# Optimization experiments

Measured on AMD Instinct MI355X. Metric: run time of the kernel, lower is better.

Reference implementation:

```python
import jax, jax.numpy as jnp
import numpy as np

N = 100000
D = 16          # input_dim
NUM_FILTERS = 8
NNZ = 1600000


def setup_inputs() -> dict:
    key = jax.random.key(0)
    k1, k2, k3, k4, k5 = jax.random.split(key, 5)
    x = jax.random.normal(k1, (N, D), dtype=jnp.float32)
    L_rows = jax.random.randint(k2, (NNZ,), 0, N, dtype=jnp.int64 if jax.config.jax_enable_x64 else jnp.int32).astype(jnp.int32)
    L_cols = jax.random.randint(k3, (NNZ,), 0, N, dtype=jnp.int32)
    L_v = jax.random.normal(k4, (NNZ,), dtype=jnp.float32)
    node_attr_eig = jax.random.uniform(k5, (N,), dtype=jnp.float32)
    return {"x": x, "L_rows": L_rows, "L_cols": L_cols, "L_v": L_v, "node_attr_eig": node_attr_eig}


def reference(x, L_rows, L_cols, L_v, node_attr_eig):
    n, d = x.shape
    f = NUM_FILTERS
    # exponents = 2 ** arange(num_filters + 1)
    exponents = (2 ** jnp.arange(f + 1)).astype(x.dtype)  # [F+1]
    # coeffs = x.T @ L  ==  (L.T @ x).T ; compute L.T @ x as [N, D]
    # (L.T @ x)[c] = sum over nnz entries (r, c): L_v * x[r]
    LTx = jax.ops.segment_sum(L_v[:, None] * x[L_rows], L_cols, num_segments=n)  # [N, D]
    # exponential eigenfilter bank: w = exp(-eig)^exponents, wavelet differences
    w = jnp.exp(-node_attr_eig)[:, None] ** exponents[None, :]  # [N, F+1]
    w_wav = w[:, :-1] - w[:, 1:]                                # [N, F]
    # g_eig = coeffs[..., None] * w_wav[None, ...] permuted to [N, D, F]
    g_eig = (LTx[:, :, None] * w_wav[:, None, :]).reshape(n, d * f)  # [N, D*F]
    # filtered = L @ g_eig : out[r] = sum over nnz (r, c): L_v * g_eig[c]
    out = jax.ops.segment_sum(L_v[:, None] * g_eig[L_cols], L_rows, num_segments=n)
    return out.reshape(n, d, f)
```

## Files before the change

kernel.cpp:

```cpp
#include <hip/hip_runtime.h>

#define N_NODES   100000
#define D_DIM     16
#define NFILT     8
#define KOUT      128
#define NNZ_CNT   1600000

#define SHIFT1    12
#define NC1       25
#define CAP1      67072
#define NSUB      64
#define CROWS     64
#define NCB       (NC1 * NSUB)
#define CAP       1408
#define EPB       2048
#define NBLKA     ((NNZ_CNT + EPB - 1) / EPB)
#define CHB       ((CAP1 + EPB - 1) / EPB)
#define CPAD      16


__device__ __forceinline__ uint f32_to_bf16_bits(float f) {
    uint u = __float_as_uint(f);
    uint r = (u + 0x7FFFu + ((u >> 16) & 1u)) >> 16;
    return r;
}

__global__ void wav_kernel(const float* __restrict__ eig, uint* __restrict__ combo) {
    int n = blockIdx.x * blockDim.x + threadIdx.x;
    if (n >= N_NODES) return;
    float cur = expf(-eig[n]);
    uint pk[4];
#pragma unroll
    for (int h = 0; h < 4; ++h) {
        float nx0 = cur * cur;
        float w0 = cur - nx0;
        float nx1 = nx0 * nx0;
        float w1 = nx0 - nx1;
        cur = nx1;
        pk[h] = f32_to_bf16_bits(w0) | (f32_to_bf16_bits(w1) << 16);
    }
    *(uint4*)(combo + (size_t)n * 16 + 8) = make_uint4(pk[0], pk[1], pk[2], pk[3]);
}

__global__ __launch_bounds__(512) void binC2_kernel(const int* __restrict__ rows,
                                                    const int* __restrict__ cols,
                                                    const float* __restrict__ v,
                                                    int* __restrict__ gc1c,
                                                    int* __restrict__ gc1r,
                                                    int2* __restrict__ regBc,
                                                    int2* __restrict__ regBr) {
    __shared__ int cnt[NC1], offb[NC1], gbase[NC1], cur[NC1];
    __shared__ int2 rec[EPB];
    __shared__ unsigned char rbk[EPB];
    int tid = threadIdx.x;
    int e0 = blockIdx.x * EPB;
    int nE = NNZ_CNT - e0; if (nE > EPB) nE = EPB;

    int r_[4], c_[4], vb_[4];
    int nk = 0;
#pragma unroll
    for (int kk = 0; kk < 4; ++kk) {
        int i = tid + kk * 512;
        if (i < nE) {
            r_[kk] = rows[e0 + i];
            c_[kk] = cols[e0 + i];
            vb_[kk] = __float_as_int(v[e0 + i]);
            nk = kk + 1;
        }
    }

    if (tid < NC1) cnt[tid] = 0;
    __syncthreads();
    for (int kk = 0; kk < nk; ++kk) atomicAdd(&cnt[c_[kk] >> SHIFT1], 1);
    __syncthreads();
    if (tid == 0) { int run = 0; for (int b = 0; b < NC1; ++b) { offb[b] = run; run += cnt[b]; } }
    __syncthreads();
    if (tid < NC1) {
        gbase[tid] = cnt[tid] ? atomicAdd(&gc1c[tid * CPAD], cnt[tid]) : 0;
        cur[tid] = offb[tid];
    }
    __syncthreads();
    for (int kk = 0; kk < nk; ++kk) {
        int b = c_[kk] >> SHIFT1;
        int pos = atomicAdd(&cur[b], 1);
        rec[pos] = make_int2(((c_[kk] & 4095) << 17) | r_[kk], vb_[kk]);
        rbk[pos] = (unsigned char)b;
    }
    __syncthreads();
    for (int i = tid; i < nE; i += 512) {
        int b = rbk[i];
        int slot = gbase[b] + (i - offb[b]);
        if (slot < CAP1) regBc[(size_t)b * CAP1 + slot] = rec[i];
    }
    __syncthreads();

    if (tid < NC1) cnt[tid] = 0;
    __syncthreads();
    for (int kk = 0; kk < nk; ++kk) atomicAdd(&cnt[r_[kk] >> SHIFT1], 1);
    __syncthreads();
    if (tid == 0) { int run = 0; for (int b = 0; b < NC1; ++b) { offb[b] = run; run += cnt[b]; } }
    __syncthreads();
    if (tid < NC1) {
        gbase[tid] = cnt[tid] ? atomicAdd(&gc1r[tid * CPAD], cnt[tid]) : 0;
        cur[tid] = offb[tid];
    }
    __syncthreads();
    for (int kk = 0; kk < nk; ++kk) {
        int b = r_[kk] >> SHIFT1;
        int pos = atomicAdd(&cur[b], 1);
        rec[pos] = make_int2(((r_[kk] & 4095) << 17) | c_[kk], vb_[kk]);
        rbk[pos] = (unsigned char)b;
    }
    __syncthreads();
    for (int i = tid; i < nE; i += 512) {
        int b = rbk[i];
        int slot = gbase[b] + (i - offb[b]);
        if (slot < CAP1) regBr[(size_t)b * CAP1 + slot] = rec[i];
    }
}

__global__ __launch_bounds__(512) void binF_kernel(const int* __restrict__ gcur1,
                                                   const int2* __restrict__ regB,
                                                   int* __restrict__ gcurF,
                                                   int2* __restrict__ regA) {
    __shared__ int cnt[NSUB], offb[NSUB], gbase[NSUB], cur[NSUB];
    __shared__ int2 rec[EPB];
    __shared__ unsigned char rbk[EPB];
    int tid = threadIdx.x;
    int cb = blockIdx.x / CHB;
    int ch = blockIdx.x % CHB;
    int nc = gcur1[cb * CPAD]; if (nc > CAP1) nc = CAP1;
    int cs = ch * EPB;
    if (cs >= nc) return;
    int nE = nc - cs; if (nE > EPB) nE = EPB;
    size_t srcb = (size_t)cb * CAP1 + cs;

    if (tid < NSUB) cnt[tid] = 0;
    __syncthreads();

    int2 my[4]; int msub[4];
    int nk = 0;
#pragma unroll
    for (int kk = 0; kk < 4; ++kk) {
        int i = tid + kk * 512;
        msub[kk] = -1;
        if (i < nE) {
            my[kk] = regB[srcb + i];
            msub[kk] = (my[kk].x >> 23) & (NSUB - 1);
            nk = kk + 1;
            atomicAdd(&cnt[msub[kk]], 1);
        }
    }
    __syncthreads();

    if (tid == 0) { int run = 0; for (int b = 0; b < NSUB; ++b) { offb[b] = run; run += cnt[b]; } }
    __syncthreads();
    if (tid < NSUB) {
        gbase[tid] = cnt[tid] ? atomicAdd(&gcurF[(cb * NSUB + tid) * CPAD], cnt[tid]) : 0;
        cur[tid] = offb[tid];
    }
    __syncthreads();

    for (int kk = 0; kk < nk; ++kk)
        if (msub[kk] >= 0) {
            int pos = atomicAdd(&cur[msub[kk]], 1);
            rec[pos] = make_int2(my[kk].x & 0x7FFFFF, my[kk].y);
            rbk[pos] = (unsigned char)msub[kk];
        }
    __syncthreads();

    for (int i = tid; i < nE; i += 512) {
        int b = rbk[i];
        int slot = gbase[b] + (i - offb[b]);
        if (slot < CAP)
            regA[(size_t)(cb * NSUB + b) * CAP + slot] = rec[i];
    }
}

__global__ __launch_bounds__(256) void sortgather1_kernel(const int* __restrict__ gcurF,
                                                          const int2* __restrict__ regA,
                                                          const float* __restrict__ x,
                                                          uint* __restrict__ combo) {
    __shared__ int2 rec[CAP];
    __shared__ int cnt[CROWS], sc[CROWS], st[CROWS], cur[CROWS];
    int tid = threadIdx.x;
    int b = blockIdx.x;
    int nb = gcurF[b * CPAD]; if (nb > CAP) nb = CAP;
    size_t base = (size_t)b * CAP;

    int2 my[6]; int mkey[6];
    if (tid < CROWS) cnt[tid] = 0;
    __syncthreads();
#pragma unroll
    for (int s = 0; s < 6; ++s) {
        int i = tid + s * 256;
        mkey[s] = -1;
        if (i < nb) {
            my[s] = regA[base + i];
            mkey[s] = my[s].x >> 17;
            atomicAdd(&cnt[mkey[s]], 1);
        }
    }
    __syncthreads();

    int cv = (tid < CROWS) ? cnt[tid] : 0;
    if (tid < CROWS) sc[tid] = cv;
    __syncthreads();
    for (int off = 1; off < CROWS; off <<= 1) {
        int t = (tid < CROWS && tid >= off) ? sc[tid - off] : 0;
        __syncthreads();
        if (tid < CROWS) sc[tid] += t;
        __syncthreads();
    }
    if (tid < CROWS) { int s0 = sc[tid] - cv; st[tid] = s0; cur[tid] = s0; }
    __syncthreads();

#pragma unroll
    for (int s = 0; s < 6; ++s)
        if (mkey[s] >= 0) {
            int pos = atomicAdd(&cur[mkey[s]], 1);
            if (pos < CAP) rec[pos] = make_int2(my[s].x & 0x1FFFF, my[s].y);
        }
    __syncthreads();

    int wave = tid >> 6, lane = tid & 63;
    int d = lane & 15, j = lane >> 4;
    for (int cl = wave; cl < CROWS; cl += 4) {
        int c = b * CROWS + cl;
        int i0 = st[cl], e0 = i0 + cnt[cl]; if (e0 > CAP) e0 = CAP;
        float acc = 0.f;
        for (int i = i0 + j; i < e0; i += 4) {
            int2 e = rec[i];
            acc = fmaf(__int_as_float(e.y), x[(size_t)e.x * D_DIM + d], acc);
        }
        acc += __shfl_xor(acc, 16);
        acc += __shfl_xor(acc, 32);
        float hi = __shfl_down(acc, 8);
        if (lane < 8 && c < N_NODES)
            combo[(size_t)c * 16 + lane] =
                f32_to_bf16_bits(acc) | (f32_to_bf16_bits(hi) << 16);
    }
}

__global__ __launch_bounds__(256) void sortgather2_kernel(const int* __restrict__ gcurF,
                                                          const int2* __restrict__ regA,
                                                          const uint* __restrict__ combo,
                                                          float* __restrict__ out) {
    __shared__ int2 rec[CAP];
    __shared__ int cnt[CROWS], sc[CROWS], st[CROWS], cur[CROWS];
    int tid = threadIdx.x;
    int b = blockIdx.x;
    int nb = gcurF[b * CPAD]; if (nb > CAP) nb = CAP;
    size_t base = (size_t)b * CAP;

    int2 my[6]; int mkey[6];
    if (tid < CROWS) cnt[tid] = 0;
    __syncthreads();
#pragma unroll
    for (int s = 0; s < 6; ++s) {
        int i = tid + s * 256;
        mkey[s] = -1;
        if (i < nb) {
            my[s] = regA[base + i];
            mkey[s] = my[s].x >> 17;
            atomicAdd(&cnt[mkey[s]], 1);
        }
    }
    __syncthreads();

    int cv = (tid < CROWS) ? cnt[tid] : 0;
    if (tid < CROWS) sc[tid] = cv;
    __syncthreads();
    for (int off = 1; off < CROWS; off <<= 1) {
        int t = (tid < CROWS && tid >= off) ? sc[tid - off] : 0;
        __syncthreads();
        if (tid < CROWS) sc[tid] += t;
        __syncthreads();
    }
    if (tid < CROWS) { int s0 = sc[tid] - cv; st[tid] = s0; cur[tid] = s0; }
    __syncthreads();

#pragma unroll
    for (int s = 0; s < 6; ++s)
        if (mkey[s] >= 0) {
            int pos = atomicAdd(&cur[mkey[s]], 1);
            if (pos < CAP) rec[pos] = make_int2(my[s].x & 0x1FFFF, my[s].y);
        }
    __syncthreads();

    int wave = tid >> 6, lane = tid & 63;
    int d0 = lane >> 3;
    int f  = lane & 7;
    for (int rl = wave; rl < CROWS; rl += 4) {
        int row = b * CROWS + rl;
        if (row >= N_NODES) continue;
        int i = st[rl], end = st[rl] + cnt[rl]; if (end > CAP) end = CAP;
        float acc0 = 0.f, acc1 = 0.f;
        for (; i + 4 <= end; i += 4) {
            int2 e0 = rec[i], e1 = rec[i + 1], e2 = rec[i + 2], e3 = rec[i + 3];
            uint l0 = combo[(size_t)e0.x * 16 + d0];
            uint l1 = combo[(size_t)e1.x * 16 + d0];
            uint l2 = combo[(size_t)e2.x * 16 + d0];
            uint l3 = combo[(size_t)e3.x * 16 + d0];
            uint w0 = ((const ushort*)(combo + (size_t)e0.x * 16 + 8))[f];
            uint w1 = ((const ushort*)(combo + (size_t)e1.x * 16 + 8))[f];
            uint w2 = ((const ushort*)(combo + (size_t)e2.x * 16 + 8))[f];
            uint w3 = ((const ushort*)(combo + (size_t)e3.x * 16 + 8))[f];
            float vw0 = __int_as_float(e0.y) * __uint_as_float(w0 << 16);
            float vw1 = __int_as_float(e1.y) * __uint_as_float(w1 << 16);
            float vw2 = __int_as_float(e2.y) * __uint_as_float(w2 << 16);
            float vw3 = __int_as_float(e3.y) * __uint_as_float(w3 << 16);
            acc0 = fmaf(vw0, __uint_as_float(l0 << 16), acc0);
            acc1 = fmaf(vw0, __uint_as_float(l0 & 0xFFFF0000u), acc1);
            acc0 = fmaf(vw1, __uint_as_float(l1 << 16), acc0);
            acc1 = fmaf(vw1, __uint_as_float(l1 & 0xFFFF0000u), acc1);
            acc0 = fmaf(vw2, __uint_as_float(l2 << 16), acc0);
            acc1 = fmaf(vw2, __uint_as_float(l2 & 0xFFFF0000u), acc1);
            acc0 = fmaf(vw3, __uint_as_float(l3 << 16), acc0);
            acc1 = fmaf(vw3, __uint_as_float(l3 & 0xFFFF0000u), acc1);
        }
        for (; i < end; ++i) {
            int2 e = rec[i];
            uint l = combo[(size_t)e.x * 16 + d0];
            uint w = ((const ushort*)(combo + (size_t)e.x * 16 + 8))[f];
            float vw = __int_as_float(e.y) * __uint_as_float(w << 16);
            acc0 = fmaf(vw, __uint_as_float(l << 16), acc0);
            acc1 = fmaf(vw, __uint_as_float(l & 0xFFFF0000u), acc1);
        }
        __builtin_nontemporal_store(acc0, &out[(size_t)row * KOUT + lane]);
        __builtin_nontemporal_store(acc1, &out[(size_t)row * KOUT + 64 + lane]);
    }
}

extern "C" void kernel_launch(void* const* d_in, const int* in_sizes, int n_in,
                              void* d_out, int out_size, void* d_ws, size_t ws_size,
                              hipStream_t stream) {
    const float* x      = (const float*)d_in[0];
    const int*   L_rows = (const int*)  d_in[1];
    const int*   L_cols = (const int*)  d_in[2];
    const float* L_v    = (const float*)d_in[3];
    const float* eig    = (const float*)d_in[4];
    float* out = (float*)d_out;

    uint* combo = (uint*)d_ws;
    int2* regBc = (int2*)(combo + (size_t)N_NODES * 16);
    int2* regBr = regBc + (size_t)NC1 * CAP1;
    int2* regA  = regBr + (size_t)NC1 * CAP1;
    int*  gc1c  = (int*)(regA + (size_t)NCB * CAP);
    int*  gc1r  = gc1c + NC1 * CPAD;
    int*  gfc   = gc1r + NC1 * CPAD;
    int*  gfr   = gfc + NCB * CPAD;

    hipMemsetAsync(gc1c, 0, (size_t)(2 * NC1 + 2 * NCB) * CPAD * sizeof(int), stream);

    wav_kernel<<<(N_NODES + 255) / 256, 256, 0, stream>>>(eig, combo);

    binC2_kernel<<<NBLKA, 512, 0, stream>>>(L_rows, L_cols, L_v, gc1c, gc1r, regBc, regBr);

    binF_kernel<<<NC1 * CHB, 512, 0, stream>>>(gc1c, regBc, gfc, regA);
    sortgather1_kernel<<<NCB, 256, 0, stream>>>(gfc, regA, x, combo);

    binF_kernel<<<NC1 * CHB, 512, 0, stream>>>(gc1r, regBr, gfr, regA);
    sortgather2_kernel<<<NCB, 256, 0, stream>>>(gfr, regA, combo, out);
}
```

Before: 260.0 us.

## Fuse wavelet into binning and co-schedule row binning with first gather

Moves the eigen-wavelet computation into the first binning kernel, removing a separate launch. It gives the column and row fine-binning passes separate scratch buffers, so the row-side fine binning can run in the same launch as the first sort-gather. That merged launch uses 512-thread blocks with a shared-memory union, which is meant to cut launch gaps and let the two independent stages overlap. It also shrinks the per-bucket capacity from 1408 to 1280, which lowers shared memory and register use but raises the risk of dropping entries if a bucket overflows.

```diff
diff --git a/kernel.cpp b/kernel.cpp
--- a/kernel.cpp
+++ b/kernel.cpp
@@ -12,11 +12,14 @@
 #define NSUB      64
 #define CROWS     64
 #define NCB       (NC1 * NSUB)
-#define CAP       1408
+#define CAP       1280
 #define EPB       2048
 #define NBLKA     ((NNZ_CNT + EPB - 1) / EPB)
 #define CHB       ((CAP1 + EPB - 1) / EPB)
+#define NBF       (NC1 * CHB)
 #define CPAD      16
+
+#define SMEM_INTS 4864
 
 
 __device__ __forceinline__ uint f32_to_bf16_bits(float f) {
@@ -25,36 +28,39 @@
     return r;
 }
 
-__global__ void wav_kernel(const float* __restrict__ eig, uint* __restrict__ combo) {
-    int n = blockIdx.x * blockDim.x + threadIdx.x;
-    if (n >= N_NODES) return;
-    float cur = expf(-eig[n]);
-    uint pk[4];
-#pragma unroll
-    for (int h = 0; h < 4; ++h) {
-        float nx0 = cur * cur;
-        float w0 = cur - nx0;
-        float nx1 = nx0 * nx0;
-        float w1 = nx0 - nx1;
-        cur = nx1;
-        pk[h] = f32_to_bf16_bits(w0) | (f32_to_bf16_bits(w1) << 16);
-    }
-    *(uint4*)(combo + (size_t)n * 16 + 8) = make_uint4(pk[0], pk[1], pk[2], pk[3]);
-}
-
 __global__ __launch_bounds__(512) void binC2_kernel(const int* __restrict__ rows,
                                                     const int* __restrict__ cols,
                                                     const float* __restrict__ v,
+                                                    const float* __restrict__ eig,
                                                     int* __restrict__ gc1c,
                                                     int* __restrict__ gc1r,
                                                     int2* __restrict__ regBc,
-                                                    int2* __restrict__ regBr) {
+                                                    int2* __restrict__ regBr,
+                                                    uint* __restrict__ combo) {
     __shared__ int cnt[NC1], offb[NC1], gbase[NC1], cur[NC1];
     __shared__ int2 rec[EPB];
     __shared__ unsigned char rbk[EPB];
     int tid = threadIdx.x;
     int e0 = blockIdx.x * EPB;
     int nE = NNZ_CNT - e0; if (nE > EPB) nE = EPB;
+
+    {
+        int n = blockIdx.x * 128 + tid;
+        if (tid < 128 && n < N_NODES) {
+            float curw = expf(-eig[n]);
+            uint pk[4];
+#pragma unroll
+            for (int h = 0; h < 4; ++h) {
+                float nx0 = curw * curw;
+                float w0 = curw - nx0;
+                float nx1 = nx0 * nx0;
+                float w1 = nx0 - nx1;
+                curw = nx1;
+                pk[h] = f32_to_bf16_bits(w0) | (f32_to_bf16_bits(w1) << 16);
+            }
+            *(uint4*)(combo + (size_t)n * 16 + 8) = make_uint4(pk[0], pk[1], pk[2], pk[3]);
+        }
+    }
 
     int r_[4], c_[4], vb_[4];
     int nk = 0;
@@ -119,16 +125,21 @@
     }
 }
 
-__global__ __launch_bounds__(512) void binF_kernel(const int* __restrict__ gcur1,
-                                                   const int2* __restrict__ regB,
-                                                   int* __restrict__ gcurF,
-                                                   int2* __restrict__ regA) {
-    __shared__ int cnt[NSUB], offb[NSUB], gbase[NSUB], cur[NSUB];
-    __shared__ int2 rec[EPB];
-    __shared__ unsigned char rbk[EPB];
+__device__ __forceinline__ void binF_body(int bfb,
+                                          const int* __restrict__ gcur1,
+                                          const int2* __restrict__ regB,
+                                          int* __restrict__ gcurF,
+                                          int2* __restrict__ regA,
+                                          int* sm) {
+    int* cnt   = sm;
+    int* offb  = sm + NSUB;
+    int* gbase = sm + 2 * NSUB;
+    int* cur   = sm + 3 * NSUB;
+    int2* rec  = (int2*)(sm + 256);
+    unsigned char* rbk = (unsigned char*)(sm + 256 + 2 * EPB);
     int tid = threadIdx.x;
-    int cb = blockIdx.x / CHB;
-    int ch = blockIdx.x % CHB;
+    int cb = bfb / CHB;
+    int ch = bfb % CHB;
     int nc = gcur1[cb * CPAD]; if (nc > CAP1) nc = CAP1;
     int cs = ch * EPB;
     if (cs >= nc) return;
@@ -177,23 +188,35 @@
     }
 }
 
-__global__ __launch_bounds__(256) void sortgather1_kernel(const int* __restrict__ gcurF,
-                                                          const int2* __restrict__ regA,
-                                                          const float* __restrict__ x,
-                                                          uint* __restrict__ combo) {
-    __shared__ int2 rec[CAP];
-    __shared__ int cnt[CROWS], sc[CROWS], st[CROWS], cur[CROWS];
+__global__ __launch_bounds__(512) void binF_kernel(const int* __restrict__ gcur1,
+                                                   const int2* __restrict__ regB,
+                                                   int* __restrict__ gcurF,
+                                                   int2* __restrict__ regA) {
+    __shared__ alignas(16) int sm[SMEM_INTS];
+    binF_body(blockIdx.x, gcur1, regB, gcurF, regA, sm);
+}
+
+__device__ __forceinline__ void sg1_body(int b,
+                                         const int* __restrict__ gcurF,
+                                         const int2* __restrict__ regA,
+                                         const float* __restrict__ x,
+                                         uint* __restrict__ combo,
+                                         int* sm) {
+    int* cnt = sm;
+    int* sc  = sm + CROWS;
+    int* st  = sm + 2 * CROWS;
+    int* cur = sm + 3 * CROWS;
+    int2* rec = (int2*)(sm + 256);
     int tid = threadIdx.x;
-    int b = blockIdx.x;
     int nb = gcurF[b * CPAD]; if (nb > CAP) nb = CAP;
     size_t base = (size_t)b * CAP;
 
-    int2 my[6]; int mkey[6];
+    int2 my[3]; int mkey[3];
     if (tid < CROWS) cnt[tid] = 0;
     __syncthreads();
 #pragma unroll
-    for (int s = 0; s < 6; ++s) {
-        int i = tid + s * 256;
+    for (int s = 0; s < 3; ++s) {
+        int i = tid + s * 512;
         mkey[s] = -1;
         if (i < nb) {
             my[s] = regA[base + i];
@@ -216,7 +239,7 @@
     __syncthreads();
 
 #pragma unroll
-    for (int s = 0; s < 6; ++s)
+    for (int s = 0; s < 3; ++s)
         if (mkey[s] >= 0) {
             int pos = atomicAdd(&cur[mkey[s]], 1);
             if (pos < CAP) rec[pos] = make_int2(my[s].x & 0x1FFFF, my[s].y);
@@ -225,7 +248,7 @@
 
     int wave = tid >> 6, lane = tid & 63;
     int d = lane & 15, j = lane >> 4;
-    for (int cl = wave; cl < CROWS; cl += 4) {
+    for (int cl = wave; cl < CROWS; cl += 8) {
         int c = b * CROWS + cl;
         int i0 = st[cl], e0 = i0 + cnt[cl]; if (e0 > CAP) e0 = CAP;
         float acc = 0.f;
@@ -240,6 +263,20 @@
             combo[(size_t)c * 16 + lane] =
                 f32_to_bf16_bits(acc) | (f32_to_bf16_bits(hi) << 16);
     }
+}
+
+__global__ __launch_bounds__(512) void binFr_sg1_kernel(const int* __restrict__ gc1r,
+                                                        const int2* __restrict__ regBr,
+                                                        int* __restrict__ gfr,
+                                                        int2* __restrict__ regAr,
+                                                        const int* __restrict__ gfc,
+                                                        const int2* __restrict__ regAc,
+                                                        const float* __restrict__ x,
+                                                        uint* __restrict__ combo) {
+    __shared__ alignas(16) int sm[SMEM_INTS];
+    int bb = blockIdx.x;
+    if (bb < NBF) binF_body(bb, gc1r, regBr, gfr, regAr, sm);
+    else          sg1_body(bb - NBF, gfc, regAc, x, combo, sm);
 }
 
 __global__ __launch_bounds__(256) void sortgather2_kernel(const int* __restrict__ gcurF,
@@ -253,11 +290,11 @@
     int nb = gcurF[b * CPAD]; if (nb > CAP) nb = CAP;
     size_t base = (size_t)b * CAP;
 
-    int2 my[6]; int mkey[6];
+    int2 my[5]; int mkey[5];
     if (tid < CROWS) cnt[tid] = 0;
     __syncthreads();
 #pragma unroll
-    for (int s = 0; s < 6; ++s) {
+    for (int s = 0; s < 5; ++s) {
         int i = tid + s * 256;
         mkey[s] = -1;
         if (i < nb) {
@@ -281,7 +318,7 @@
     __syncthreads();
 
 #pragma unroll
-    for (int s = 0; s < 6; ++s)
+    for (int s = 0; s < 5; ++s)
         if (mkey[s] >= 0) {
             int pos = atomicAdd(&cur[mkey[s]], 1);
             if (pos < CAP) rec[pos] = make_int2(my[s].x & 0x1FFFF, my[s].y);
@@ -345,21 +382,22 @@
     uint* combo = (uint*)d_ws;
     int2* regBc = (int2*)(combo + (size_t)N_NODES * 16);
     int2* regBr = regBc + (size_t)NC1 * CAP1;
-    int2* regA  = regBr + (size_t)NC1 * CAP1;
-    int*  gc1c  = (int*)(regA + (size_t)NCB * CAP);
+    int2* regAc = regBr + (size_t)NC1 * CAP1;
+    int2* regAr = regAc + (size_t)NCB * CAP;
+    int*  gc1c  = (int*)(regAr + (size_t)NCB * CAP);
     int*  gc1r  = gc1c + NC1 * CPAD;
     int*  gfc   = gc1r + NC1 * CPAD;
     int*  gfr   = gfc + NCB * CPAD;
 
     hipMemsetAsync(gc1c, 0, (size_t)(2 * NC1 + 2 * NCB) * CPAD * sizeof(int), stream);
 
-    wav_kernel<<<(N_NODES + 255) / 256, 256, 0, stream>>>(eig, combo);
-
-    binC2_kernel<<<NBLKA, 512, 0, stream>>>(L_rows, L_cols, L_v, gc1c, gc1r, regBc, regBr);
-
-    binF_kernel<<<NC1 * CHB, 512, 0, stream>>>(gc1c, regBc, gfc, regA);
-    sortgather1_kernel<<<NCB, 256, 0, stream>>>(gfc, regA, x, combo);
-
-    binF_kernel<<<NC1 * CHB, 512, 0, stream>>>(gc1r, regBr, gfr, regA);
-    sortgather2_kernel<<<NCB, 256, 0, stream>>>(gfr, regA, combo, out);
-}
+    binC2_kernel<<<NBLKA, 512, 0, stream>>>(L_rows, L_cols, L_v, eig,
+                                            gc1c, gc1r, regBc, regBr, combo);
+
+    binF_kernel<<<NBF, 512, 0, stream>>>(gc1c, regBc, gfc, regAc);
+
+    binFr_sg1_kernel<<<NBF + NCB, 512, 0, stream>>>(gc1r, regBr, gfr, regAr,
+                                                    gfc, regAc, x, combo);
+
+    sortgather2_kernel<<<NCB, 256, 0, stream>>>(gfr, regAr, combo, out);
+}
```

Result: slower. 276.7 us (+6.4%).

## Use per-wave histograms in binning and replace sort-gather with shared-atomic accumulation

Applied to the files above, without the earlier changes.

The first binning kernel now builds a separate shared-memory histogram and scatter cursor for each wave, which cuts contention on the 25 shared counters. The first gather kernel no longer sorts edges by column inside the block. It accumulates each edge's contribution directly into a shared 64x16 float buffer with shared atomics, then packs the result to bf16. This removes the count, scan and scatter passes, but adds float atomic traffic and makes the summation order nondeterministic.

```diff
diff --git a/kernel.cpp b/kernel.cpp
--- a/kernel.cpp
+++ b/kernel.cpp
@@ -16,6 +16,7 @@
 #define EPB       2048
 #define NBLKA     ((NNZ_CNT + EPB - 1) / EPB)
 #define CHB       ((CAP1 + EPB - 1) / EPB)
+#define NWAVES    8
 #define CPAD      16
 
 
@@ -49,10 +50,12 @@
                                                     int* __restrict__ gc1r,
                                                     int2* __restrict__ regBc,
                                                     int2* __restrict__ regBr) {
-    __shared__ int cnt[NC1], offb[NC1], gbase[NC1], cur[NC1];
+    __shared__ int hist[NWAVES * NC1];
+    __shared__ int cnt[NC1], offb[NC1], gbase[NC1];
     __shared__ int2 rec[EPB];
     __shared__ unsigned char rbk[EPB];
     int tid = threadIdx.x;
+    int wv = tid >> 6;
     int e0 = blockIdx.x * EPB;
     int nE = NNZ_CNT - e0; if (nE > EPB) nE = EPB;
 
@@ -69,20 +72,32 @@
         }
     }
 
-    if (tid < NC1) cnt[tid] = 0;
-    __syncthreads();
-    for (int kk = 0; kk < nk; ++kk) atomicAdd(&cnt[c_[kk] >> SHIFT1], 1);
+    for (int i = tid; i < NWAVES * NC1; i += 512) hist[i] = 0;
+    __syncthreads();
+    for (int kk = 0; kk < nk; ++kk)
+        atomicAdd(&hist[wv * NC1 + (c_[kk] >> SHIFT1)], 1);
+    __syncthreads();
+    if (tid < NC1) {
+        int tot = 0;
+        for (int w = 0; w < NWAVES; ++w) tot += hist[w * NC1 + tid];
+        cnt[tid] = tot;
+    }
     __syncthreads();
     if (tid == 0) { int run = 0; for (int b = 0; b < NC1; ++b) { offb[b] = run; run += cnt[b]; } }
     __syncthreads();
     if (tid < NC1) {
         gbase[tid] = cnt[tid] ? atomicAdd(&gc1c[tid * CPAD], cnt[tid]) : 0;
-        cur[tid] = offb[tid];
+        int run = offb[tid];
+        for (int w = 0; w < NWAVES; ++w) {
+            int h = hist[w * NC1 + tid];
+            hist[w * NC1 + tid] = run;
+            run += h;
+        }
     }
     __syncthreads();
     for (int kk = 0; kk < nk; ++kk) {
         int b = c_[kk] >> SHIFT1;
-        int pos = atomicAdd(&cur[b], 1);
+        int pos = atomicAdd(&hist[wv * NC1 + b], 1);
         rec[pos] = make_int2(((c_[kk] & 4095) << 17) | r_[kk], vb_[kk]);
         rbk[pos] = (unsigned char)b;
     }
@@ -94,20 +109,32 @@
     }
     __syncthreads();
 
-    if (tid < NC1) cnt[tid] = 0;
-    __syncthreads();
-    for (int kk = 0; kk < nk; ++kk) atomicAdd(&cnt[r_[kk] >> SHIFT1], 1);
+    for (int i = tid; i < NWAVES * NC1; i += 512) hist[i] = 0;
+    __syncthreads();
+    for (int kk = 0; kk < nk; ++kk)
+        atomicAdd(&hist[wv * NC1 + (r_[kk] >> SHIFT1)], 1);
+    __syncthreads();
+    if (tid < NC1) {
+        int tot = 0;
+        for (int w = 0; w < NWAVES; ++w) tot += hist[w * NC1 + tid];
+        cnt[tid] = tot;
+    }
     __syncthreads();
     if (tid == 0) { int run = 0; for (int b = 0; b < NC1; ++b) { offb[b] = run; run += cnt[b]; } }
     __syncthreads();
     if (tid < NC1) {
         gbase[tid] = cnt[tid] ? atomicAdd(&gc1r[tid * CPAD], cnt[tid]) : 0;
-        cur[tid] = offb[tid];
+        int run = offb[tid];
+        for (int w = 0; w < NWAVES; ++w) {
+            int h = hist[w * NC1 + tid];
+            hist[w * NC1 + tid] = run;
+            run += h;
+        }
     }
     __syncthreads();
     for (int kk = 0; kk < nk; ++kk) {
         int b = r_[kk] >> SHIFT1;
-        int pos = atomicAdd(&cur[b], 1);
+        int pos = atomicAdd(&hist[wv * NC1 + b], 1);
         rec[pos] = make_int2(((r_[kk] & 4095) << 17) | c_[kk], vb_[kk]);
         rbk[pos] = (unsigned char)b;
     }
@@ -177,68 +204,40 @@
     }
 }
 
-__global__ __launch_bounds__(256) void sortgather1_kernel(const int* __restrict__ gcurF,
-                                                          const int2* __restrict__ regA,
-                                                          const float* __restrict__ x,
-                                                          uint* __restrict__ combo) {
+__global__ __launch_bounds__(256) void sg1_nosort_kernel(const int* __restrict__ gcurF,
+                                                         const int2* __restrict__ regA,
+                                                         const float* __restrict__ x,
+                                                         uint* __restrict__ combo) {
+    __shared__ float acc[CROWS * D_DIM];
     __shared__ int2 rec[CAP];
-    __shared__ int cnt[CROWS], sc[CROWS], st[CROWS], cur[CROWS];
     int tid = threadIdx.x;
     int b = blockIdx.x;
     int nb = gcurF[b * CPAD]; if (nb > CAP) nb = CAP;
     size_t base = (size_t)b * CAP;
 
-    int2 my[6]; int mkey[6];
-    if (tid < CROWS) cnt[tid] = 0;
-    __syncthreads();
-#pragma unroll
-    for (int s = 0; s < 6; ++s) {
-        int i = tid + s * 256;
-        mkey[s] = -1;
-        if (i < nb) {
-            my[s] = regA[base + i];
-            mkey[s] = my[s].x >> 17;
-            atomicAdd(&cnt[mkey[s]], 1);
-        }
-    }
-    __syncthreads();
-
-    int cv = (tid < CROWS) ? cnt[tid] : 0;
-    if (tid < CROWS) sc[tid] = cv;
-    __syncthreads();
-    for (int off = 1; off < CROWS; off <<= 1) {
-        int t = (tid < CROWS && tid >= off) ? sc[tid - off] : 0;
-        __syncthreads();
-        if (tid < CROWS) sc[tid] += t;
-        __syncthreads();
-    }
-    if (tid < CROWS) { int s0 = sc[tid] - cv; st[tid] = s0; cur[tid] = s0; }
-    __syncthreads();
-
-#pragma unroll
-    for (int s = 0; s < 6; ++s)
-        if (mkey[s] >= 0) {
-            int pos = atomicAdd(&cur[mkey[s]], 1);
-            if (pos < CAP) rec[pos] = make_int2(my[s].x & 0x1FFFF, my[s].y);
-        }
-    __syncthreads();
-
-    int wave = tid >> 6, lane = tid & 63;
-    int d = lane & 15, j = lane >> 4;
-    for (int cl = wave; cl < CROWS; cl += 4) {
+    for (int t = tid; t < CROWS * D_DIM; t += 256) acc[t] = 0.f;
+    for (int i = tid; i < nb; i += 256) rec[i] = regA[base + i];
+    __syncthreads();
+
+    int wv = tid >> 6, lane = tid & 63;
+    int sub = lane >> 4;
+    int d = lane & 15;
+    for (int i = (wv << 2) + sub; i < nb; i += 16) {
+        int2 e = rec[i];
+        int cl = e.x >> 17;
+        int r  = e.x & 0x1FFFF;
+        atomicAdd(&acc[(cl << 4) + d],
+                  __int_as_float(e.y) * x[(size_t)r * D_DIM + d]);
+    }
+    __syncthreads();
+
+    for (int t = tid; t < CROWS * NFILT; t += 256) {
+        int cl = t >> 3, j = t & 7;
         int c = b * CROWS + cl;
-        int i0 = st[cl], e0 = i0 + cnt[cl]; if (e0 > CAP) e0 = CAP;
-        float acc = 0.f;
-        for (int i = i0 + j; i < e0; i += 4) {
-            int2 e = rec[i];
-            acc = fmaf(__int_as_float(e.y), x[(size_t)e.x * D_DIM + d], acc);
-        }
-        acc += __shfl_xor(acc, 16);
-        acc += __shfl_xor(acc, 32);
-        float hi = __shfl_down(acc, 8);
-        if (lane < 8 && c < N_NODES)
-            combo[(size_t)c * 16 + lane] =
-                f32_to_bf16_bits(acc) | (f32_to_bf16_bits(hi) << 16);
+        if (c < N_NODES)
+            combo[(size_t)c * 16 + j] =
+                f32_to_bf16_bits(acc[(cl << 4) + j]) |
+                (f32_to_bf16_bits(acc[(cl << 4) + j + 8]) << 16);
     }
 }
 
@@ -358,7 +357,7 @@
     binC2_kernel<<<NBLKA, 512, 0, stream>>>(L_rows, L_cols, L_v, gc1c, gc1r, regBc, regBr);
 
     binF_kernel<<<NC1 * CHB, 512, 0, stream>>>(gc1c, regBc, gfc, regA);
-    sortgather1_kernel<<<NCB, 256, 0, stream>>>(gfc, regA, x, combo);
+    sg1_nosort_kernel<<<NCB, 256, 0, stream>>>(gfc, regA, x, combo);
 
     binF_kernel<<<NC1 * CHB, 512, 0, stream>>>(gc1r, regBr, gfr, regA);
     sortgather2_kernel<<<NCB, 256, 0, stream>>>(gfr, regA, combo, out);
```

New measurement: 376.0 us. +44.6%, slower.

## Use per-wave shared histograms in binning and split combo buffer into separate arrays

Applied to the files above, without the earlier changes.

The first binning kernel now keeps one histogram per wave and prefix-scans it per wave. Only 25 buckets are shared among 512 threads, so the single shared histogram's atomics were heavily contended; per-wave copies reduce that. The interleaved 64-byte combo record (LTx plus wavelet weights) is also split into two contiguous arrays, LTxP (32 B per node) and wavb (16 B per node). This changes the gather access pattern in the second sort-gather kernel, which may touch two cache lines per neighbor instead of one.

```diff
diff --git a/kernel.cpp b/kernel.cpp
--- a/kernel.cpp
+++ b/kernel.cpp
@@ -16,8 +16,8 @@
 #define EPB       2048
 #define NBLKA     ((NNZ_CNT + EPB - 1) / EPB)
 #define CHB       ((CAP1 + EPB - 1) / EPB)
+#define NWAVES    8
 #define CPAD      16
-
 
 __device__ __forceinline__ uint f32_to_bf16_bits(float f) {
     uint u = __float_as_uint(f);
@@ -25,7 +25,7 @@
     return r;
 }
 
-__global__ void wav_kernel(const float* __restrict__ eig, uint* __restrict__ combo) {
+__global__ void wav_kernel(const float* __restrict__ eig, ushort* __restrict__ wavb) {
     int n = blockIdx.x * blockDim.x + threadIdx.x;
     if (n >= N_NODES) return;
     float cur = expf(-eig[n]);
@@ -39,7 +39,7 @@
         cur = nx1;
         pk[h] = f32_to_bf16_bits(w0) | (f32_to_bf16_bits(w1) << 16);
     }
-    *(uint4*)(combo + (size_t)n * 16 + 8) = make_uint4(pk[0], pk[1], pk[2], pk[3]);
+    *(uint4*)(wavb + (size_t)n * NFILT) = make_uint4(pk[0], pk[1], pk[2], pk[3]);
 }
 
 __global__ __launch_bounds__(512) void binC2_kernel(const int* __restrict__ rows,
@@ -49,10 +49,12 @@
                                                     int* __restrict__ gc1r,
                                                     int2* __restrict__ regBc,
                                                     int2* __restrict__ regBr) {
-    __shared__ int cnt[NC1], offb[NC1], gbase[NC1], cur[NC1];
+    __shared__ int hist[NWAVES * NC1];
+    __shared__ int cnt[NC1], offb[NC1], gbase[NC1];
     __shared__ int2 rec[EPB];
     __shared__ unsigned char rbk[EPB];
     int tid = threadIdx.x;
+    int wv = tid >> 6;
     int e0 = blockIdx.x * EPB;
     int nE = NNZ_CNT - e0; if (nE > EPB) nE = EPB;
 
@@ -69,20 +71,32 @@
         }
     }
 
-    if (tid < NC1) cnt[tid] = 0;
-    __syncthreads();
-    for (int kk = 0; kk < nk; ++kk) atomicAdd(&cnt[c_[kk] >> SHIFT1], 1);
+    for (int i = tid; i < NWAVES * NC1; i += 512) hist[i] = 0;
+    __syncthreads();
+    for (int kk = 0; kk < nk; ++kk)
+        atomicAdd(&hist[wv * NC1 + (c_[kk] >> SHIFT1)], 1);
+    __syncthreads();
+    if (tid < NC1) {
+        int tot = 0;
+        for (int w = 0; w < NWAVES; ++w) tot += hist[w * NC1 + tid];
+        cnt[tid] = tot;
+    }
     __syncthreads();
     if (tid == 0) { int run = 0; for (int b = 0; b < NC1; ++b) { offb[b] = run; run += cnt[b]; } }
     __syncthreads();
     if (tid < NC1) {
         gbase[tid] = cnt[tid] ? atomicAdd(&gc1c[tid * CPAD], cnt[tid]) : 0;
-        cur[tid] = offb[tid];
+        int run = offb[tid];
+        for (int w = 0; w < NWAVES; ++w) {
+            int h = hist[w * NC1 + tid];
+            hist[w * NC1 + tid] = run;
+            run += h;
+        }
     }
     __syncthreads();
     for (int kk = 0; kk < nk; ++kk) {
         int b = c_[kk] >> SHIFT1;
-        int pos = atomicAdd(&cur[b], 1);
+        int pos = atomicAdd(&hist[wv * NC1 + b], 1);
         rec[pos] = make_int2(((c_[kk] & 4095) << 17) | r_[kk], vb_[kk]);
         rbk[pos] = (unsigned char)b;
     }
@@ -94,20 +108,32 @@
     }
     __syncthreads();
 
-    if (tid < NC1) cnt[tid] = 0;
-    __syncthreads();
-    for (int kk = 0; kk < nk; ++kk) atomicAdd(&cnt[r_[kk] >> SHIFT1], 1);
+    for (int i = tid; i < NWAVES * NC1; i += 512) hist[i] = 0;
+    __syncthreads();
+    for (int kk = 0; kk < nk; ++kk)
+        atomicAdd(&hist[wv * NC1 + (r_[kk] >> SHIFT1)], 1);
+    __syncthreads();
+    if (tid < NC1) {
+        int tot = 0;
+        for (int w = 0; w < NWAVES; ++w) tot += hist[w * NC1 + tid];
+        cnt[tid] = tot;
+    }
     __syncthreads();
     if (tid == 0) { int run = 0; for (int b = 0; b < NC1; ++b) { offb[b] = run; run += cnt[b]; } }
     __syncthreads();
     if (tid < NC1) {
         gbase[tid] = cnt[tid] ? atomicAdd(&gc1r[tid * CPAD], cnt[tid]) : 0;
-        cur[tid] = offb[tid];
+        int run = offb[tid];
+        for (int w = 0; w < NWAVES; ++w) {
+            int h = hist[w * NC1 + tid];
+            hist[w * NC1 + tid] = run;
+            run += h;
+        }
     }
     __syncthreads();
     for (int kk = 0; kk < nk; ++kk) {
         int b = r_[kk] >> SHIFT1;
-        int pos = atomicAdd(&cur[b], 1);
+        int pos = atomicAdd(&hist[wv * NC1 + b], 1);
         rec[pos] = make_int2(((r_[kk] & 4095) << 17) | c_[kk], vb_[kk]);
         rbk[pos] = (unsigned char)b;
     }
@@ -180,7 +206,7 @@
 __global__ __launch_bounds__(256) void sortgather1_kernel(const int* __restrict__ gcurF,
                                                           const int2* __restrict__ regA,
                                                           const float* __restrict__ x,
-                                                          uint* __restrict__ combo) {
+                                                          uint* __restrict__ LTxP) {
     __shared__ int2 rec[CAP];
     __shared__ int cnt[CROWS], sc[CROWS], st[CROWS], cur[CROWS];
     int tid = threadIdx.x;
@@ -237,14 +263,15 @@
         acc += __shfl_xor(acc, 32);
         float hi = __shfl_down(acc, 8);
         if (lane < 8 && c < N_NODES)
-            combo[(size_t)c * 16 + lane] =
+            LTxP[(size_t)c * NFILT + lane] =
                 f32_to_bf16_bits(acc) | (f32_to_bf16_bits(hi) << 16);
     }
 }
 
 __global__ __launch_bounds__(256) void sortgather2_kernel(const int* __restrict__ gcurF,
                                                           const int2* __restrict__ regA,
-                                                          const uint* __restrict__ combo,
+                                                          const uint* __restrict__ LTxP,
+                                                          const ushort* __restrict__ wavb,
                                                           float* __restrict__ out) {
     __shared__ int2 rec[CAP];
     __shared__ int cnt[CROWS], sc[CROWS], st[CROWS], cur[CROWS];
@@ -298,14 +325,14 @@
         float acc0 = 0.f, acc1 = 0.f;
         for (; i + 4 <= end; i += 4) {
             int2 e0 = rec[i], e1 = rec[i + 1], e2 = rec[i + 2], e3 = rec[i + 3];
-            uint l0 = combo[(size_t)e0.x * 16 + d0];
-            uint l1 = combo[(size_t)e1.x * 16 + d0];
-            uint l2 = combo[(size_t)e2.x * 16 + d0];
-            uint l3 = combo[(size_t)e3.x * 16 + d0];
-            uint w0 = ((const ushort*)(combo + (size_t)e0.x * 16 + 8))[f];
-            uint w1 = ((const ushort*)(combo + (size_t)e1.x * 16 + 8))[f];
-            uint w2 = ((const ushort*)(combo + (size_t)e2.x * 16 + 8))[f];
-            uint w3 = ((const ushort*)(combo + (size_t)e3.x * 16 + 8))[f];
+            uint l0 = LTxP[e0.x * NFILT + d0];
+            uint l1 = LTxP[e1.x * NFILT + d0];
+            uint l2 = LTxP[e2.x * NFILT + d0];
+            uint l3 = LTxP[e3.x * NFILT + d0];
+            uint w0 = wavb[e0.x * NFILT + f];
+            uint w1 = wavb[e1.x * NFILT + f];
+            uint w2 = wavb[e2.x * NFILT + f];
+            uint w3 = wavb[e3.x * NFILT + f];
             float vw0 = __int_as_float(e0.y) * __uint_as_float(w0 << 16);
             float vw1 = __int_as_float(e1.y) * __uint_as_float(w1 << 16);
             float vw2 = __int_as_float(e2.y) * __uint_as_float(w2 << 16);
@@ -321,8 +348,8 @@
         }
         for (; i < end; ++i) {
             int2 e = rec[i];
-            uint l = combo[(size_t)e.x * 16 + d0];
-            uint w = ((const ushort*)(combo + (size_t)e.x * 16 + 8))[f];
+            uint l = LTxP[e.x * NFILT + d0];
+            uint w = wavb[e.x * NFILT + f];
             float vw = __int_as_float(e.y) * __uint_as_float(w << 16);
             acc0 = fmaf(vw, __uint_as_float(l << 16), acc0);
             acc1 = fmaf(vw, __uint_as_float(l & 0xFFFF0000u), acc1);
@@ -342,24 +369,25 @@
     const float* eig    = (const float*)d_in[4];
     float* out = (float*)d_out;
 
-    uint* combo = (uint*)d_ws;
-    int2* regBc = (int2*)(combo + (size_t)N_NODES * 16);
-    int2* regBr = regBc + (size_t)NC1 * CAP1;
-    int2* regA  = regBr + (size_t)NC1 * CAP1;
-    int*  gc1c  = (int*)(regA + (size_t)NCB * CAP);
-    int*  gc1r  = gc1c + NC1 * CPAD;
-    int*  gfc   = gc1r + NC1 * CPAD;
-    int*  gfr   = gfc + NCB * CPAD;
+    uint*   LTxP = (uint*)d_ws;
+    ushort* wavb = (ushort*)(LTxP + (size_t)N_NODES * NFILT);
+    int2*   regBc = (int2*)(wavb + (size_t)N_NODES * NFILT);
+    int2*   regBr = regBc + (size_t)NC1 * CAP1;
+    int2*   regA  = regBr + (size_t)NC1 * CAP1;
+    int*    gc1c  = (int*)(regA + (size_t)NCB * CAP);
+    int*    gc1r  = gc1c + NC1 * CPAD;
+    int*    gfc   = gc1r + NC1 * CPAD;
+    int*    gfr   = gfc + NCB * CPAD;
 
     hipMemsetAsync(gc1c, 0, (size_t)(2 * NC1 + 2 * NCB) * CPAD * sizeof(int), stream);
 
-    wav_kernel<<<(N_NODES + 255) / 256, 256, 0, stream>>>(eig, combo);
+    wav_kernel<<<(N_NODES + 255) / 256, 256, 0, stream>>>(eig, wavb);
 
     binC2_kernel<<<NBLKA, 512, 0, stream>>>(L_rows, L_cols, L_v, gc1c, gc1r, regBc, regBr);
 
     binF_kernel<<<NC1 * CHB, 512, 0, stream>>>(gc1c, regBc, gfc, regA);
-    sortgather1_kernel<<<NCB, 256, 0, stream>>>(gfc, regA, x, combo);
+    sortgather1_kernel<<<NCB, 256, 0, stream>>>(gfc, regA, x, LTxP);
 
     binF_kernel<<<NC1 * CHB, 512, 0, stream>>>(gc1r, regBr, gfr, regA);
-    sortgather2_kernel<<<NCB, 256, 0, stream>>>(gfr, regA, combo, out);
-}
+    sortgather2_kernel<<<NCB, 256, 0, stream>>>(gfr, regA, LTxP, wavb, out);
+}
```

New measurement: 284.8 us. 9.5% more time.
